# Kernel tuning notes

Hardware: AMD Instinct MI355X
Metric: run time of the kernel (lower is better)

## Reference

```python
import jax, jax.numpy as jnp
import numpy as np

B, D, K = 512, 128, 131072
TEMP = 0.07
PTR = 0  # queue_ptr starts at 0; B <= K so single contiguous write


def _normalize(x, axis):
    return x / jnp.linalg.norm(x, axis=axis, keepdims=True)


def setup_inputs() -> dict:
    key = jax.random.key(0)
    k = jax.random.split(key, 7)
    return {
        "predict0": jax.random.normal(k[0], (B, D), jnp.float32),
        "predict1": jax.random.normal(k[1], (B, D), jnp.float32),
        "project0": jax.random.normal(k[2], (B, D), jnp.float32),
        "project1": jax.random.normal(k[3], (B, D), jnp.float32),
        "queue": jax.random.normal(k[4], (D, K), jnp.float32),
        "queue_id": jax.random.randint(k[5], (K,), 0, 100000, jnp.int64) if jax.config.jax_enable_x64 else jax.random.randint(k[5], (K,), 0, 100000, jnp.int32),
        "ids": jax.random.randint(k[6], (B,), 0, 100000, jnp.int64) if jax.config.jax_enable_x64 else jax.random.randint(k[6], (B,), 0, 100000, jnp.int32),
    }


def _find_nn(proj, queue_n, queue_id, ids):
    # [B, K] similarity, mask out entries with same sample id, argmax, gather cols
    sim = proj @ queue_n                                   # [B, K]
    is_own = queue_id[None, :] == ids[:, None]             # [B, K]
    sim = jnp.where(is_own, jnp.float32(-1.0), sim)
    idx = jnp.argmax(sim, axis=1)                          # [B]
    return queue_n[:, idx]                                 # [D, B]


def _nnclr_loss(predicted, nn, temperature):
    # logits[i, j] = nn_i . predicted_j / T ; labels = arange(B)
    logits = (nn.T @ predicted.T) / temperature            # [B, B]
    logp = jax.nn.log_softmax(logits, axis=-1)
    return -jnp.mean(jnp.diagonal(logp))


def reference(predict0, predict1, project0, project1, queue, queue_id, ids):
    # forward_encoder's normalization (encoder itself is external and modeled out)
    p0 = _normalize(predict0, 1)
    p1 = _normalize(predict1, 1)
    z0 = _normalize(project0, 1)
    z1 = _normalize(project1, 1)
    queue_n = _normalize(queue, 0)  # queue stored normalized along dim 0

    # find_nn / queue are no_grad in the original
    nn0 = jax.lax.stop_gradient(_find_nn(jax.lax.stop_gradient(z0), queue_n, queue_id, ids))
    nn1 = jax.lax.stop_gradient(_find_nn(jax.lax.stop_gradient(z1), queue_n, queue_id, ids))

    loss0 = _nnclr_loss(p0, nn1, TEMP)
    loss1 = _nnclr_loss(p1, nn0, TEMP)
    loss = (loss0 + loss1) * 0.5

    # _dequeue_and_enqueue: ptr=0, B <= K -> contiguous slice write
    new_queue = jax.lax.dynamic_update_slice(queue_n, jax.lax.stop_gradient(z0.T), (0, PTR))
    new_queue_id = jax.lax.dynamic_update_slice(queue_id, ids, (PTR,))
    new_ptr = jnp.array((PTR + B) % K, dtype=queue_id.dtype)
    return loss, new_queue, new_queue_id, new_ptr
```

## Files before the change

### kernel.cpp

```cpp
#include <hip/hip_runtime.h>
#include <hip/hip_bf16.h>

typedef _Float16 half8 __attribute__((ext_vector_type(8)));
typedef _Float16 half4 __attribute__((ext_vector_type(4)));
typedef float f32x4 __attribute__((ext_vector_type(4)));

#define B 512
#define D 128
#define K 131072
#define TEMP 0.07f
#define NKB 512
#define KT_PER 16

#define INVN_OFF 0
#define Z0_OFF   131072
#define Z1_OFF   196608
#define P0_OFF   262144
#define P1_OFF   327680
#define ZF16_OFF 393216
#define QA_OFF   458752
#define PVAL_OFF 8847360
#define WKB_OFF  9371648
#define WVAL_OFF 9372672
#define IDX_OFF  9373696
#define LP_OFF   9374720

__global__ __launch_bounds__(128) void rownorm_k(
    const float* __restrict__ p0, const float* __restrict__ p1,
    const float* __restrict__ z0, const float* __restrict__ z1,
    float* __restrict__ w, _Float16* __restrict__ zf16) {
  int row = blockIdx.x & (B - 1);
  int which = blockIdx.x >> 9;
  const float* src; float* dst;
  switch (which) {
    case 0: src = z0; dst = w + Z0_OFF; break;
    case 1: src = z1; dst = w + Z1_OFF; break;
    case 2: src = p0; dst = w + P0_OFF; break;
    default: src = p1; dst = w + P1_OFF; break;
  }
  int tid = threadIdx.x;
  float v = src[row * D + tid];
  float s = v * v;
  #pragma unroll
  for (int o = 32; o; o >>= 1) s += __shfl_xor(s, o);
  __shared__ float sm[2];
  if ((tid & 63) == 0) sm[tid >> 6] = s;
  __syncthreads();
  float inv = rsqrtf(sm[0] + sm[1]);
  float nv = v * inv;
  dst[row * D + tid] = nv;
  if (which < 2) zf16[(which * B + row) * D + tid] = (_Float16)nv;
}

__global__ __launch_bounds__(256) void colq_k(
    const float* __restrict__ q, const int* __restrict__ qid,
    const int* __restrict__ ids, const float* __restrict__ w_z0,
    float* __restrict__ invn, float* __restrict__ out,
    _Float16* __restrict__ qA) {
  __shared__ float psum[8][128];
  __shared__ float invs[128];
  __shared__ _Float16 tile[128][136];
  int tid = threadIdx.x;
  int kb = blockIdx.x;
  int k0 = kb * 128;
  {
    int kc = tid & 31, dg = tid >> 5;
    float4 acc = {0.f, 0.f, 0.f, 0.f};
    for (int i = 0; i < 16; i++) {
      int d = dg * 16 + i;
      float4 v = *(const float4*)(q + (size_t)d * K + k0 + kc * 4);
      acc.x = fmaf(v.x, v.x, acc.x); acc.y = fmaf(v.y, v.y, acc.y);
      acc.z = fmaf(v.z, v.z, acc.z); acc.w = fmaf(v.w, v.w, acc.w);
    }
    *(float4*)&psum[dg][kc * 4] = acc;
  }
  __syncthreads();
  if (tid < 128) {
    float s = 0.f;
    #pragma unroll
    for (int g2 = 0; g2 < 8; g2++) s += psum[g2][tid];
    float inv = rsqrtf(s);
    invs[tid] = inv;
    invn[k0 + tid] = inv;
    int kk = k0 + tid;
    out[1 + (size_t)D * K + kk] = (float)((kk < B) ? ids[kk] : qid[kk]);
  }
  __syncthreads();
  {
    int col = tid & 127, dh = tid >> 7;
    float inv = invs[col];
    const float* qc = q + k0 + col;
    float* oc = out + 1 + k0 + col;
    if (k0 < B) {
      const float* zc = w_z0 + (size_t)(k0 + col) * D;
      for (int i = 0; i < 64; i++) {
        int d = dh * 64 + i;
        float o = qc[(size_t)d * K] * inv;
        tile[d][col] = (_Float16)o;
        oc[(size_t)d * K] = zc[d];
      }
    } else {
      for (int i = 0; i < 64; i++) {
        int d = dh * 64 + i;
        float o = qc[(size_t)d * K] * inv;
        tile[d][col] = (_Float16)o;
        oc[(size_t)d * K] = o;
      }
    }
  }
  __syncthreads();
  {
    int dc = tid >> 6, l = tid & 63;
    int g = l >> 4, c = l & 15;
    #pragma unroll
    for (int kt = 0; kt < 8; kt++) {
      half8 f;
      #pragma unroll
      for (int i = 0; i < 8; i++) {
        int d = g * 4 + (i & 3) + ((i >> 2) << 4) + dc * 32;
        f[i] = tile[d][kt * 16 + c];
      }
      int ktg = kb * 8 + kt;
      *(half8*)(qA + (size_t)((ktg * 4 + dc) * 64 + l) * 8) = f;
    }
  }
}

#define LOADAF(AF, Q4, KTG) do { \
  _Pragma("unroll") \
  for (int dc = 0; dc < 4; dc++) \
    AF[dc] = *(const half8*)(qA + (size_t)(((KTG) * 4 + dc) * 64 + lane) * 8); \
  Q4 = *(const int4*)(qid + (KTG) * 16 + g * 4); \
} while (0)

#define PROCESS(AF, Q4, KTG) do { \
  _Pragma("unroll") \
  for (int nt = 0; nt < 4; nt++) { \
    f32x4 acc = {0.f, 0.f, 0.f, 0.f}; \
    _Pragma("unroll") \
    for (int dc = 0; dc < 4; dc++) \
      acc = __builtin_amdgcn_mfma_f32_16x16x32_f16(AF[dc], bf[nt][dc], acc, 0, 0, 0); \
    _Pragma("unroll") \
    for (int r = 0; r < 4; r++) { \
      int qv_ = (r == 0) ? Q4.x : (r == 1) ? Q4.y : (r == 2) ? Q4.z : Q4.w; \
      float sm_ = (qv_ == myid[nt]) ? -1.0f : acc[r]; \
      best[nt] = fmaxf(best[nt], sm_); \
    } \
  } \
} while (0)

__global__ __launch_bounds__(256) void nnsearch_k(
    const _Float16* __restrict__ qA, const _Float16* __restrict__ zf16,
    const int* __restrict__ qid, const int* __restrict__ ids,
    float* __restrict__ pval) {
  int tid = threadIdx.x;
  int kb = blockIdx.x;
  int rg = blockIdx.y;
  int wave = tid >> 6, lane = tid & 63;
  int g = lane >> 4, c = lane & 15;
  int rowbase = rg * 256 + wave * 64;

  half8 bf[4][4];
  int myid[4];
  #pragma unroll
  for (int nt = 0; nt < 4; nt++) {
    int row = rowbase + nt * 16 + c;
    myid[nt] = ids[row & (B - 1)];
    #pragma unroll
    for (int dc = 0; dc < 4; dc++) {
      const _Float16* zr = zf16 + row * D + dc * 32 + g * 4;
      half4 lo = *(const half4*)zr;
      half4 hi = *(const half4*)(zr + 16);
      half8 f = {lo[0], lo[1], lo[2], lo[3], hi[0], hi[1], hi[2], hi[3]};
      bf[nt][dc] = f;
    }
  }

  float best[4] = {-2.f, -2.f, -2.f, -2.f};
  int kt0 = kb * KT_PER;
  half8 afA[4], afB[4];
  int4 q4A, q4B;
  LOADAF(afA, q4A, kt0);
  for (int kt = 0; kt < KT_PER; kt += 2) {
    LOADAF(afB, q4B, kt0 + kt + 1);
    PROCESS(afA, q4A, kt0 + kt);
    if (kt + 2 < KT_PER) LOADAF(afA, q4A, kt0 + kt + 2);
    PROCESS(afB, q4B, kt0 + kt + 1);
  }

  #pragma unroll
  for (int nt = 0; nt < 4; nt++) {
    float v = best[nt];
    v = fmaxf(v, __shfl_xor(v, 16));
    v = fmaxf(v, __shfl_xor(v, 32));
    if (g == 0) {
      int row = rowbase + nt * 16 + c;
      pval[row * NKB + kb] = v;
    }
  }
}

__global__ __launch_bounds__(256) void nnreduce_k(
    const float* __restrict__ pval, int* __restrict__ wkb,
    float* __restrict__ wval) {
  int row = blockIdx.x;
  int tid = threadIdx.x;
  const float* p = pval + row * NKB;
  float a = p[tid], b = p[tid + 256];
  unsigned pa = (__float_as_uint(fmaf(a, 0.5f, 3.0f)) << 9) | (unsigned)(511 - tid);
  unsigned pb = (__float_as_uint(fmaf(b, 0.5f, 3.0f)) << 9) | (unsigned)(255 - tid);
  unsigned v = pa > pb ? pa : pb;
  #pragma unroll
  for (int o = 32; o; o >>= 1) {
    unsigned ov = __shfl_xor(v, o);
    v = v > ov ? v : ov;
  }
  __shared__ unsigned sv[4];
  if ((tid & 63) == 0) sv[tid >> 6] = v;
  __syncthreads();
  if (tid == 0) {
    #pragma unroll
    for (int wv = 1; wv < 4; wv++) v = v > sv[wv] ? v : sv[wv];
    int kb = 511 - (int)(v & 0x1FFu);
    wkb[row] = kb;
    wval[row] = pval[row * NKB + kb];
  }
}

__global__ __launch_bounds__(256) void nnfix_k(
    const _Float16* __restrict__ qA, const _Float16* __restrict__ zf16,
    const int* __restrict__ qid, const int* __restrict__ ids,
    const int* __restrict__ wkb, const float* __restrict__ wval,
    int* __restrict__ idxout) {
  int tid = threadIdx.x;
  int wave = tid >> 6, lane = tid & 63;
  int g = lane >> 4;
  int row = blockIdx.x * 4 + wave;
  int kb = wkb[row];
  float wv = wval[row];
  int myid = ids[row & (B - 1)];

  half8 bf[4];
  #pragma unroll
  for (int dc = 0; dc < 4; dc++) {
    const _Float16* zr = zf16 + row * D + dc * 32 + g * 4;
    half4 lo = *(const half4*)zr;
    half4 hi = *(const half4*)(zr + 16);
    half8 f = {lo[0], lo[1], lo[2], lo[3], hi[0], hi[1], hi[2], hi[3]};
    bf[dc] = f;
  }

  unsigned kbest = 0x7FFFFFFFu;
  int kt0 = kb * KT_PER;
  for (int kt = 0; kt < KT_PER; kt++) {
    int ktg = kt0 + kt;
    half8 af[4];
    #pragma unroll
    for (int dc = 0; dc < 4; dc++)
      af[dc] = *(const half8*)(qA + (size_t)((ktg * 4 + dc) * 64 + lane) * 8);
    int4 q4 = *(const int4*)(qid + ktg * 16 + g * 4);
    f32x4 acc = {0.f, 0.f, 0.f, 0.f};
    #pragma unroll
    for (int dc = 0; dc < 4; dc++)
      acc = __builtin_amdgcn_mfma_f32_16x16x32_f16(af[dc], bf[dc], acc, 0, 0, 0);
    #pragma unroll
    for (int r = 0; r < 4; r++) {
      int qv = (r == 0) ? q4.x : (r == 1) ? q4.y : (r == 2) ? q4.z : q4.w;
      float sm = (qv == myid) ? -1.0f : acc[r];
      if (sm == wv) {
        unsigned kk = (unsigned)(ktg * 16 + g * 4 + r);
        kbest = kbest < kk ? kbest : kk;
      }
    }
  }
  unsigned o1 = __shfl_xor(kbest, 16); kbest = kbest < o1 ? kbest : o1;
  unsigned o2 = __shfl_xor(kbest, 32); kbest = kbest < o2 ? kbest : o2;
  if (lane == 0) idxout[row] = (int)(kbest < (K - 1) ? kbest : (K - 1));
}

__global__ __launch_bounds__(256) void loss_k(
    const float* __restrict__ q, const float* __restrict__ invn,
    const int* __restrict__ idxout, const float* __restrict__ w,
    float* __restrict__ lpart) {
  int i0 = blockIdx.x * 8;
  int v = blockIdx.y;
  int tid = threadIdx.x;
  __shared__ float nns[8][D];
  __shared__ float rm[8][4], re[8][4], sdlds[8];
  #pragma unroll
  for (int ii = 0; ii < 4; ii++) {
    int i = ii * 2 + (tid >> 7);
    int d = tid & 127;
    int nnidx = idxout[(v ? 0 : B) + i0 + i];
    nns[i][d] = q[(size_t)d * K + nnidx] * invn[nnidx];
  }
  __syncthreads();
  const float* pr = w + (v ? P1_OFF : P0_OFF);
  const float* r0 = pr + tid * D;
  const float* r1 = pr + (tid + 256) * D;
  float a0[8] = {0, 0, 0, 0, 0, 0, 0, 0};
  float a1[8] = {0, 0, 0, 0, 0, 0, 0, 0};
  for (int d = 0; d < D; d += 4) {
    float4 x0 = *(const float4*)(r0 + d);
    float4 x1 = *(const float4*)(r1 + d);
    #pragma unroll
    for (int i = 0; i < 8; i++) {
      float4 n = *(const float4*)&nns[i][d];
      a0[i] = fmaf(x0.x, n.x, a0[i]); a0[i] = fmaf(x0.y, n.y, a0[i]);
      a0[i] = fmaf(x0.z, n.z, a0[i]); a0[i] = fmaf(x0.w, n.w, a0[i]);
      a1[i] = fmaf(x1.x, n.x, a1[i]); a1[i] = fmaf(x1.y, n.y, a1[i]);
      a1[i] = fmaf(x1.z, n.z, a1[i]); a1[i] = fmaf(x1.w, n.w, a1[i]);
    }
  }
  #pragma unroll
  for (int i = 0; i < 8; i++) {
    a0[i] *= (1.0f / TEMP);
    a1[i] *= (1.0f / TEMP);
  }
  #pragma unroll
  for (int i = 0; i < 8; i++) {
    int ig = i0 + i;
    if ((ig & 256) == 0) { if (tid == ig) sdlds[i] = a0[i]; }
    else { if (tid == (ig & 255)) sdlds[i] = a1[i]; }
  }
  int wv = tid >> 6;
  #pragma unroll
  for (int i = 0; i < 8; i++) {
    float m = fmaxf(a0[i], a1[i]);
    #pragma unroll
    for (int o = 32; o; o >>= 1) m = fmaxf(m, __shfl_xor(m, o));
    if ((tid & 63) == 0) rm[i][wv] = m;
  }
  __syncthreads();
  #pragma unroll
  for (int i = 0; i < 8; i++) {
    float m = fmaxf(fmaxf(rm[i][0], rm[i][1]), fmaxf(rm[i][2], rm[i][3]));
    float e = expf(a0[i] - m) + expf(a1[i] - m);
    #pragma unroll
    for (int o = 32; o; o >>= 1) e += __shfl_xor(e, o);
    if ((tid & 63) == 0) re[i][wv] = e;
  }
  __syncthreads();
  if (tid < 8) {
    int i = tid;
    float m = fmaxf(fmaxf(rm[i][0], rm[i][1]), fmaxf(rm[i][2], rm[i][3]));
    float s = re[i][0] + re[i][1] + re[i][2] + re[i][3];
    lpart[v * B + i0 + i] = sdlds[i] - m - logf(s);
  }
}

__global__ __launch_bounds__(256) void final_k(
    const float* __restrict__ lpart, float* __restrict__ out) {
  int tid = threadIdx.x;
  float s = lpart[tid] + lpart[tid + 256] + lpart[tid + 512] + lpart[tid + 768];
  #pragma unroll
  for (int o = 32; o; o >>= 1) s += __shfl_xor(s, o);
  __shared__ float sm[4];
  if ((tid & 63) == 0) sm[tid >> 6] = s;
  __syncthreads();
  if (tid == 0) {
    float total = sm[0] + sm[1] + sm[2] + sm[3];
    out[0] = -total * (1.0f / 1024.0f);
    out[1 + D * K + K] = 512.0f;
  }
}

extern "C" void kernel_launch(void* const* d_in, const int* in_sizes, int n_in,
                              void* d_out, int out_size, void* d_ws, size_t ws_size,
                              hipStream_t stream) {
  const float* p0 = (const float*)d_in[0];
  const float* p1 = (const float*)d_in[1];
  const float* z0 = (const float*)d_in[2];
  const float* z1 = (const float*)d_in[3];
  const float* q  = (const float*)d_in[4];
  const int* qid  = (const int*)d_in[5];
  const int* ids  = (const int*)d_in[6];
  float* out = (float*)d_out;
  float* w = (float*)d_ws;
  float* invn = w + INVN_OFF;
  _Float16* zf16 = (_Float16*)(w + ZF16_OFF);
  _Float16* qA   = (_Float16*)(w + QA_OFF);
  float* pval = w + PVAL_OFF;
  int* wkb    = (int*)(w + WKB_OFF);
  float* wval = w + WVAL_OFF;
  int* idxout = (int*)(w + IDX_OFF);
  float* lpart = w + LP_OFF;

  rownorm_k<<<2048, 128, 0, stream>>>(p0, p1, z0, z1, w, zf16);
  colq_k<<<K / 128, 256, 0, stream>>>(q, qid, ids, w + Z0_OFF, invn, out, qA);
  dim3 g(NKB, 4);
  nnsearch_k<<<g, 256, 0, stream>>>(qA, zf16, qid, ids, pval);
  nnreduce_k<<<1024, 256, 0, stream>>>(pval, wkb, wval);
  nnfix_k<<<256, 256, 0, stream>>>(qA, zf16, qid, ids, wkb, wval, idxout);
  dim3 gl(B / 8, 2);
  loss_k<<<gl, 256, 0, stream>>>(q, invn, idxout, w, lpart);
  final_k<<<1, 256, 0, stream>>>(lpart, out);
}
```

Before: 135.2 us.

## Vectorize colq pass, remap nnsearch block order, deepen A-fragment prefetch

The colq kernel's second pass now reads the queue with float4 loads in the same coalesced pattern as the norm pass and writes half4 tile entries, instead of scalar per-column strided loads. The nnsearch grid is flattened to 1D and blocks are remapped so the four row groups sharing a K-block run close together, which should improve L2 reuse of qA tiles, possibly also spreading work across XCDs. The A-fragment prefetch depth goes from double to quadruple buffering to hide more load latency, at the cost of more registers. The z0 overwrite path for the first blocks now does uncoalesced scalar gathers from w_z0, but only for four blocks.

```diff
diff --git a/kernel.cpp b/kernel.cpp
--- a/kernel.cpp
+++ b/kernel.cpp
@@ -63,8 +63,8 @@
   int tid = threadIdx.x;
   int kb = blockIdx.x;
   int k0 = kb * 128;
+  int kc = tid & 31, dg = tid >> 5;
   {
-    int kc = tid & 31, dg = tid >> 5;
     float4 acc = {0.f, 0.f, 0.f, 0.f};
     for (int i = 0; i < 16; i++) {
       int d = dg * 16 + i;
@@ -87,24 +87,23 @@
   }
   __syncthreads();
   {
-    int col = tid & 127, dh = tid >> 7;
-    float inv = invs[col];
-    const float* qc = q + k0 + col;
-    float* oc = out + 1 + k0 + col;
-    if (k0 < B) {
-      const float* zc = w_z0 + (size_t)(k0 + col) * D;
-      for (int i = 0; i < 64; i++) {
-        int d = dh * 64 + i;
-        float o = qc[(size_t)d * K] * inv;
-        tile[d][col] = (_Float16)o;
-        oc[(size_t)d * K] = zc[d];
-      }
-    } else {
-      for (int i = 0; i < 64; i++) {
-        int d = dh * 64 + i;
-        float o = qc[(size_t)d * K] * inv;
-        tile[d][col] = (_Float16)o;
-        oc[(size_t)d * K] = o;
+    bool zblk = (k0 < B);
+    float4 iv = *(const float4*)&invs[kc * 4];
+    for (int i = 0; i < 16; i++) {
+      int d = i * 8 + dg;
+      float4 v = *(const float4*)(q + (size_t)d * K + k0 + kc * 4);
+      float o0 = v.x * iv.x, o1 = v.y * iv.y, o2 = v.z * iv.z, o3 = v.w * iv.w;
+      half4 t = {(_Float16)o0, (_Float16)o1, (_Float16)o2, (_Float16)o3};
+      *(half4*)&tile[d][kc * 4] = t;
+      float* oc = out + 1 + (size_t)d * K + k0 + kc * 4;
+      if (zblk) {
+        int col = k0 + kc * 4;
+        oc[0] = w_z0[(size_t)(col + 0) * D + d];
+        oc[1] = w_z0[(size_t)(col + 1) * D + d];
+        oc[2] = w_z0[(size_t)(col + 2) * D + d];
+        oc[3] = w_z0[(size_t)(col + 3) * D + d];
+      } else {
+        oc[0] = o0; oc[1] = o1; oc[2] = o2; oc[3] = o3;
       }
     }
   }
@@ -154,8 +153,10 @@
     const int* __restrict__ qid, const int* __restrict__ ids,
     float* __restrict__ pval) {
   int tid = threadIdx.x;
-  int kb = blockIdx.x;
-  int rg = blockIdx.y;
+  int flat = blockIdx.x;
+  int cls = flat & 7;
+  int kb = cls * 64 + (flat >> 5);
+  int rg = (flat >> 3) & 3;
   int wave = tid >> 6, lane = tid & 63;
   int g = lane >> 4, c = lane & 15;
   int rowbase = rg * 256 + wave * 64;
@@ -178,14 +179,20 @@
 
   float best[4] = {-2.f, -2.f, -2.f, -2.f};
   int kt0 = kb * KT_PER;
-  half8 afA[4], afB[4];
-  int4 q4A, q4B;
-  LOADAF(afA, q4A, kt0);
-  for (int kt = 0; kt < KT_PER; kt += 2) {
-    LOADAF(afB, q4B, kt0 + kt + 1);
-    PROCESS(afA, q4A, kt0 + kt);
-    if (kt + 2 < KT_PER) LOADAF(afA, q4A, kt0 + kt + 2);
-    PROCESS(afB, q4B, kt0 + kt + 1);
+  half8 af0[4], af1[4], af2[4], af3[4];
+  int4 q40, q41, q42, q43;
+  LOADAF(af0, q40, kt0 + 0);
+  LOADAF(af1, q41, kt0 + 1);
+  LOADAF(af2, q42, kt0 + 2);
+  for (int kt = 0; kt < KT_PER; kt += 4) {
+    LOADAF(af3, q43, kt0 + kt + 3);
+    PROCESS(af0, q40, kt0 + kt);
+    if (kt + 4 < KT_PER) LOADAF(af0, q40, kt0 + kt + 4);
+    PROCESS(af1, q41, kt0 + kt + 1);
+    if (kt + 5 < KT_PER) LOADAF(af1, q41, kt0 + kt + 5);
+    PROCESS(af2, q42, kt0 + kt + 2);
+    if (kt + 6 < KT_PER) LOADAF(af2, q42, kt0 + kt + 6);
+    PROCESS(af3, q43, kt0 + kt + 3);
   }
 
   #pragma unroll
@@ -388,8 +395,7 @@
 
   rownorm_k<<<2048, 128, 0, stream>>>(p0, p1, z0, z1, w, zf16);
   colq_k<<<K / 128, 256, 0, stream>>>(q, qid, ids, w + Z0_OFF, invn, out, qA);
-  dim3 g(NKB, 4);
-  nnsearch_k<<<g, 256, 0, stream>>>(qA, zf16, qid, ids, pval);
+  nnsearch_k<<<2048, 256, 0, stream>>>(qA, zf16, qid, ids, pval);
   nnreduce_k<<<1024, 256, 0, stream>>>(pval, wkb, wval);
   nnfix_k<<<256, 256, 0, stream>>>(qA, zf16, qid, ids, wkb, wval, idxout);
   dim3 gl(B / 8, 2);
```

After: 154.2 us. 1.14x slower.
